# Performance work log

Measured on AMD Instinct MI355X. Metric: run time of the kernel, lower is better.

## Reference

```python
import jax, jax.numpy as jnp
import numpy as np

N, K, D = 262144, 1024, 64

def setup_inputs() -> dict:
    key = jax.random.key(0)
    kx, kc = jax.random.split(key)
    x = jax.random.normal(kx, (N, D), dtype=jnp.float32)
    centers = jax.random.normal(kc, (K, D), dtype=jnp.float32)
    return {"x": x, "centers": centers}

def reference(x, centers):
    # centers_norm is precomputed as a buffer in the torch module: (centers**2).sum(-1)
    centers_norm = jnp.sum(centers * centers, axis=-1)           # [K]
    x_norm = jnp.sum(x * x, axis=-1)                             # [N]
    dist = x_norm[..., None] - 2.0 * (x @ centers.T) + centers_norm  # [N,K]
    return jnp.argmin(jnp.abs(dist), axis=-1)                    # [N] int ids
```

## Files before the change

kernel.cpp:

```cpp
#include <hip/hip_runtime.h>
#include <float.h>


#define N_PTS 262144
#define K_CTR 1024
#define DIM   64
#define CTILE 128
#define OFFC  32.0f
#define TAU_DIST 0.05f

#define WS_CN    0
#define WS_CI    4096
#define WS_HI    8192
#define WS_LO    139264
#define WS_CTR   270336
#define WS_LIST  270592
#define WS_MIN   (270592 + 4 * 65536)

typedef __attribute__((ext_vector_type(8))) short  short8;
typedef __attribute__((ext_vector_type(8))) __bf16 bf16x8;
typedef __attribute__((ext_vector_type(4))) float  f32x4;

union FragU { short8 s; bf16x8 b; unsigned short u[8]; };

static __device__ __forceinline__ unsigned short bfbits(__bf16 h) {
    return __builtin_bit_cast(unsigned short, h);
}

#if defined(__has_builtin)
#if __has_builtin(__builtin_amdgcn_global_load_lds)
#define HAVE_GLD 1
#endif
#endif

#ifdef HAVE_GLD
#define GLD16(gsrc, ldst)                                                      \
    __builtin_amdgcn_global_load_lds(                                          \
        (const __attribute__((address_space(1))) void*)(gsrc),                 \
        (__attribute__((address_space(3))) void*)(ldst), 16, 0, 0)
#endif

__global__ void prep_kernel(const float* __restrict__ centers,
                            float* __restrict__ cn, float* __restrict__ ci,
                            int* __restrict__ counter) {
    int k = blockIdx.x * 256 + threadIdx.x;
    if (k == 0) *counter = 0;
    if (k < K_CTR) {
        const float4* c = reinterpret_cast<const float4*>(centers + (size_t)k * DIM);
        float s0 = 0.f, s1 = 0.f, s2 = 0.f, s3 = 0.f;
#pragma unroll
        for (int j = 0; j < 16; ++j) {
            float4 v = c[j];
            s0 = fmaf(v.x, v.x, s0); s1 = fmaf(v.y, v.y, s1);
            s2 = fmaf(v.z, v.z, s2); s3 = fmaf(v.w, v.w, s3);
        }
        float n = (s0 + s1) + (s2 + s3);
        cn[k] = n;
        ci[k] = fmaf(-0.5f, n, -OFFC);
    }
}

__global__ void split_kernel(const float* __restrict__ centers,
                             unsigned short* __restrict__ hiG,
                             unsigned short* __restrict__ loG) {
    int si = blockIdx.x * 256 + threadIdx.x;
    int rlow = si & 15, gg = (si >> 4) & 3, s = (si >> 6) & 1;
    int rowblk = (si >> 7) & 7, ct = si >> 10;
    int row = ct * CTILE + rowblk * 16 + rlow;
    const float* g = centers + (size_t)row * DIM + s * 32 + gg * 8;
    float4 v0 = *reinterpret_cast<const float4*>(g);
    float4 v1 = *reinterpret_cast<const float4*>(g + 4);
    float vv[8] = {v0.x, v0.y, v0.z, v0.w, v1.x, v1.y, v1.z, v1.w};
    FragU hi, lo;
#pragma unroll
    for (int j = 0; j < 8; ++j) {
        __bf16 h = (__bf16)vv[j];
        hi.u[j] = bfbits(h);
        lo.u[j] = bfbits((__bf16)(vv[j] - (float)h));
    }
    *reinterpret_cast<short8*>(hiG + (size_t)si * 8) = hi.s;
    *reinterpret_cast<short8*>(loG + (size_t)si * 8) = lo.s;
}

__launch_bounds__(256, 4)
__global__ void assign_mfma(const float* __restrict__ x,
                            const unsigned short* __restrict__ hiG,
                            const unsigned short* __restrict__ loG,
                            const float* __restrict__ ci,
                            int* __restrict__ out,
                            int* __restrict__ counter,
                            int* __restrict__ list, int cap) {
    __shared__ __align__(16) unsigned short lh[1024 * 8];
    __shared__ __align__(16) unsigned short ll[1024 * 8];
    __shared__ __align__(16) float ciL[K_CTR];

    const int tid  = threadIdx.x;
    const int wv   = tid >> 6;
    const int lane = tid & 63;
    const int g    = lane >> 4;
    const int lr   = lane & 15;
    const int pbase = blockIdx.x * 256 + wv * 64;

#pragma unroll
    for (int j = 0; j < 4; ++j) ciL[j * 256 + tid] = ci[j * 256 + tid];

    bf16x8 bh[4][2], bl[4][2];
#pragma unroll
    for (int cb = 0; cb < 4; ++cb) {
        const int p = pbase + cb * 16 + lr;
        const float* xr = x + (size_t)p * DIM + g * 8;
        float4 v0 = *reinterpret_cast<const float4*>(xr);
        float4 v1 = *reinterpret_cast<const float4*>(xr + 4);
        float4 v2 = *reinterpret_cast<const float4*>(xr + 32);
        float4 v3 = *reinterpret_cast<const float4*>(xr + 36);
        float vv[16] = {v0.x, v0.y, v0.z, v0.w, v1.x, v1.y, v1.z, v1.w,
                        v2.x, v2.y, v2.z, v2.w, v3.x, v3.y, v3.z, v3.w};
#pragma unroll
        for (int j = 0; j < 16; ++j) {
            __bf16 hb = (__bf16)vv[j];
            bh[cb][j >> 3][j & 7] = hb;
            bl[cb][j >> 3][j & 7] = (__bf16)(vv[j] - (float)hb);
        }
    }

    unsigned int best[4], sec[4];
#pragma unroll
    for (int cb = 0; cb < 4; ++cb) { best[cb] = 0xFFFFFFFFu; sec[cb] = 0xFFFFFFFFu; }

    const char* lhb = (const char*)lh + lane * 16;
    const char* llb = (const char*)ll + lane * 16;

#pragma unroll 1
    for (int ct = 0; ct < K_CTR / CTILE; ++ct) {
        __syncthreads();
        {
            const size_t sbase = (size_t)(ct * 1024 + wv * 64 + lane) * 8;
#ifdef HAVE_GLD
#pragma unroll
            for (int j = 0; j < 4; ++j) {
                GLD16(hiG + sbase + j * 256 * 8, lh + (j * 256 + wv * 64) * 8);
                GLD16(loG + sbase + j * 256 * 8, ll + (j * 256 + wv * 64) * 8);
            }
#else
            const short8* hs = reinterpret_cast<const short8*>(hiG + (size_t)ct * 1024 * 8);
            const short8* ls = reinterpret_cast<const short8*>(loG + (size_t)ct * 1024 * 8);
            short8* hd = reinterpret_cast<short8*>(lh);
            short8* ld = reinterpret_cast<short8*>(ll);
#pragma unroll
            for (int j = 0; j < 4; ++j) hd[j * 256 + tid] = hs[j * 256 + tid];
#pragma unroll
            for (int j = 0; j < 4; ++j) ld[j * 256 + tid] = ls[j * 256 + tid];
#endif
        }
        __syncthreads();

        const unsigned int ibct = ct * CTILE + g * 4;
        const float* cibase = ciL + ct * CTILE + g * 4;

#pragma unroll
        for (int st = 0; st < CTILE / 16; ++st) {
            FragU ah0, ah1, al0, al1;
            ah0.s = *reinterpret_cast<const short8*>(lhb + (st * 2 + 0) * 1024);
            ah1.s = *reinterpret_cast<const short8*>(lhb + (st * 2 + 1) * 1024);
            al0.s = *reinterpret_cast<const short8*>(llb + (st * 2 + 0) * 1024);
            al1.s = *reinterpret_cast<const short8*>(llb + (st * 2 + 1) * 1024);
            const f32x4 init4 = *reinterpret_cast<const f32x4*>(cibase + st * 16);

            f32x4 acc[4];
#pragma unroll
            for (int cb = 0; cb < 4; ++cb)
                acc[cb] = __builtin_amdgcn_mfma_f32_16x16x32_bf16(ah0.b, bh[cb][0], init4, 0, 0, 0);
#pragma unroll
            for (int cb = 0; cb < 4; ++cb)
                acc[cb] = __builtin_amdgcn_mfma_f32_16x16x32_bf16(ah0.b, bl[cb][0], acc[cb], 0, 0, 0);
#pragma unroll
            for (int cb = 0; cb < 4; ++cb)
                acc[cb] = __builtin_amdgcn_mfma_f32_16x16x32_bf16(al0.b, bh[cb][0], acc[cb], 0, 0, 0);
#pragma unroll
            for (int cb = 0; cb < 4; ++cb)
                acc[cb] = __builtin_amdgcn_mfma_f32_16x16x32_bf16(ah1.b, bh[cb][1], acc[cb], 0, 0, 0);
#pragma unroll
            for (int cb = 0; cb < 4; ++cb)
                acc[cb] = __builtin_amdgcn_mfma_f32_16x16x32_bf16(ah1.b, bl[cb][1], acc[cb], 0, 0, 0);
#pragma unroll
            for (int cb = 0; cb < 4; ++cb)
                acc[cb] = __builtin_amdgcn_mfma_f32_16x16x32_bf16(al1.b, bh[cb][1], acc[cb], 0, 0, 0);

            unsigned int vidx[4];
            vidx[0] = ibct + st * 16;
            vidx[1] = vidx[0] + 1; vidx[2] = vidx[0] + 2; vidx[3] = vidx[0] + 3;

#pragma unroll
            for (int cb = 0; cb < 4; ++cb) {
#pragma unroll
                for (int pr = 0; pr < 2; ++pr) {
                    unsigned int ka = (__float_as_uint(acc[cb][pr * 2 + 0]) & 0xFFFFFC00u) | vidx[pr * 2 + 0];
                    unsigned int kb = (__float_as_uint(acc[cb][pr * 2 + 1]) & 0xFFFFFC00u) | vidx[pr * 2 + 1];
                    unsigned int bo = best[cb], med, bn;
                    asm("v_med3_u32 %0, %1, %2, %3" : "=v"(med) : "v"(ka), "v"(kb), "v"(bo));
                    asm("v_min3_u32 %0, %1, %2, %3" : "=v"(bn)  : "v"(ka), "v"(kb), "v"(bo));
                    best[cb] = bn;
                    sec[cb]  = min(sec[cb], med);
                }
            }
        }
    }

#pragma unroll
    for (int cb = 0; cb < 4; ++cb) {
        unsigned int b = best[cb], s = sec[cb];
#pragma unroll
        for (int off = 16; off <= 32; off <<= 1) {
            unsigned int ob = __shfl_xor(b, off);
            unsigned int os = __shfl_xor(s, off);
            s = min(min(s, os), max(b, ob));
            b = min(b, ob);
        }
        if (g == 0) {
            const int p = pbase + cb * 16 + lr;
            out[p] = (int)(b & 1023u);
            float bf = __uint_as_float(b & 0xFFFFFC00u);
            float sf = __uint_as_float(s & 0xFFFFFC00u);
            if ((b < 0x80000000u) || (2.f * (bf - sf) < TAU_DIST)) {
                int sl = atomicAdd(counter, 1);
                if (sl < cap) list[sl] = p;
            }
        }
    }
}

__launch_bounds__(256, 2)
__global__ void refine2_kernel(const float* __restrict__ x,
                               const float* __restrict__ centers,
                               const float* __restrict__ cn,
                               const int* __restrict__ list,
                               const int* __restrict__ counter,
                               int* __restrict__ out, int cap) {
    __shared__ float ldsC[64 * 65];
    int cnt = *counter; if (cnt > cap) cnt = cap;
    const int tid  = threadIdx.x;
    const int wv   = tid >> 6;
    const int lane = tid & 63;

#pragma unroll 1
    for (int base = blockIdx.x * 4; base < cnt; base += gridDim.x * 4) {
        const int i = base + wv;
        const bool valid = (i < cnt);
        const int p = valid ? list[i] : 0;

        const float4* xr = reinterpret_cast<const float4*>(x + (size_t)p * DIM);
        float4 xv[16];
        float xn0 = 0.f, xn1 = 0.f, xn2 = 0.f, xn3 = 0.f;
#pragma unroll
        for (int j = 0; j < 16; ++j) {
            float4 v = xr[j]; xv[j] = v;
            xn0 = fmaf(v.x, v.x, xn0); xn1 = fmaf(v.y, v.y, xn1);
            xn2 = fmaf(v.z, v.z, xn2); xn3 = fmaf(v.w, v.w, xn3);
        }
        const float xnv = (xn0 + xn1) + (xn2 + xn3);

        float bestv = 3.4e38f; int bi = 0;
#pragma unroll 1
        for (int t = 0; t < 16; ++t) {
            __syncthreads();
#pragma unroll
            for (int j = 0; j < 16; ++j) {
                int idx = j * 256 + tid;
                int row = idx >> 6, col = idx & 63;
                ldsC[row * 65 + col] = centers[((size_t)t * 64 + row) * DIM + col];
            }
            __syncthreads();
            if (valid) {
                const int k = t * 64 + lane;
                const float* cr = ldsC + lane * 65;
                float a0 = 0.f, a1 = 0.f, a2 = 0.f, a3 = 0.f;
#pragma unroll
                for (int jj = 0; jj < 16; ++jj) {
                    a0 = fmaf(xv[jj].x, cr[jj * 4 + 0], a0);
                    a1 = fmaf(xv[jj].y, cr[jj * 4 + 1], a1);
                    a2 = fmaf(xv[jj].z, cr[jj * 4 + 2], a2);
                    a3 = fmaf(xv[jj].w, cr[jj * 4 + 3], a3);
                }
                float dot  = (a0 + a1) + (a2 + a3);
                float dist = fabsf(fmaf(-2.f, dot, xnv + cn[k]));
                if (dist < bestv) { bestv = dist; bi = k; }
            }
        }
#pragma unroll
        for (int off = 1; off < 64; off <<= 1) {
            float ob = __shfl_xor(bestv, off);
            int   oi = __shfl_xor(bi, off);
            bool take = (ob < bestv) || (ob == bestv && oi < bi);
            bestv = take ? ob : bestv;
            bi    = take ? oi : bi;
        }
        if (valid && lane == 0) out[p] = bi;
    }
}

#define TK 128
__launch_bounds__(256, 4)
__global__ void assign_fp32(const float* __restrict__ x,
                            const float* __restrict__ centers,
                            const float* __restrict__ cn,
                            int* __restrict__ out) {
    __shared__ float ldsC[TK * DIM];
    __shared__ float ldsN[TK];
    const int tid = threadIdx.x;
    const int p = blockIdx.x * 256 + tid;
    const float4* xr = reinterpret_cast<const float4*>(x + (size_t)p * DIM);
    float4 xv[16];
    float xn0 = 0.f, xn1 = 0.f, xn2 = 0.f, xn3 = 0.f;
#pragma unroll
    for (int j = 0; j < 16; ++j) {
        float4 v = xr[j]; xv[j] = v;
        xn0 = fmaf(v.x, v.x, xn0); xn1 = fmaf(v.y, v.y, xn1);
        xn2 = fmaf(v.z, v.z, xn2); xn3 = fmaf(v.w, v.w, xn3);
    }
    const float xn = (xn0 + xn1) + (xn2 + xn3);
    float bestv = 3.4e38f; int best = 0;
#pragma unroll 1
    for (int t = 0; t < K_CTR / TK; ++t) {
        __syncthreads();
        const float4* cg = reinterpret_cast<const float4*>(centers + (size_t)t * TK * DIM);
        float4* cl = reinterpret_cast<float4*>(ldsC);
#pragma unroll
        for (int j = 0; j < (TK * DIM / 4) / 256; ++j)
            cl[j * 256 + tid] = cg[j * 256 + tid];
        if (tid < TK) ldsN[tid] = cn[t * TK + tid];
        __syncthreads();
        for (int k = 0; k < TK; ++k) {
            const float4* cv = reinterpret_cast<const float4*>(ldsC + k * DIM);
            float a0 = 0.f, a1 = 0.f, a2 = 0.f, a3 = 0.f;
#pragma unroll
            for (int j = 0; j < 16; ++j) {
                float4 c4 = cv[j];
                a0 = fmaf(xv[j].x, c4.x, a0); a1 = fmaf(xv[j].y, c4.y, a1);
                a2 = fmaf(xv[j].z, c4.z, a2); a3 = fmaf(xv[j].w, c4.w, a3);
            }
            float dot = (a0 + a1) + (a2 + a3);
            float dist = fabsf(fmaf(-2.f, dot, xn + ldsN[k]));
            if (dist < bestv) { bestv = dist; best = t * TK + k; }
        }
    }
    out[p] = best;
}

extern "C" void kernel_launch(void* const* d_in, const int* in_sizes, int n_in,
                              void* d_out, int out_size, void* d_ws, size_t ws_size,
                              hipStream_t stream) {
    const float* x = (const float*)d_in[0];
    const float* centers = (const float*)d_in[1];
    int* out = (int*)d_out;
    char* ws = (char*)d_ws;
    float* cn = (float*)(ws + WS_CN);
    float* ci = (float*)(ws + WS_CI);
    unsigned short* hiG = (unsigned short*)(ws + WS_HI);
    unsigned short* loG = (unsigned short*)(ws + WS_LO);
    int* counter = (int*)(ws + WS_CTR);
    int* list = (int*)(ws + WS_LIST);

    if (ws_size >= WS_MIN) {
        size_t avail = (ws_size - WS_LIST) / sizeof(int);
        int cap = (int)(avail < (size_t)N_PTS ? avail : (size_t)N_PTS);
        prep_kernel<<<4, 256, 0, stream>>>(centers, cn, ci, counter);
        split_kernel<<<32, 256, 0, stream>>>(centers, hiG, loG);
        assign_mfma<<<N_PTS / 256, 256, 0, stream>>>(x, hiG, loG, ci, out, counter, list, cap);
        refine2_kernel<<<1024, 256, 0, stream>>>(x, centers, cn, list, counter, out, cap);
    } else {
        prep_kernel<<<4, 256, 0, stream>>>(centers, cn, ci, counter);
        assign_fp32<<<N_PTS / 256, 256, 0, stream>>>(x, centers, cn, out);
    }
}
```

Before: 120.1 us.

## Double-buffer center tiles in LDS and raise MFMA wave priority

Halves the center tile to 64 rows and double-buffers the hi/lo bf16 fragments in shared memory, so the next tile is fetched while the current one feeds the MFMAs. This drops one barrier per iteration and overlaps global-to-LDS loads with compute. It also wraps the MFMA block in s_setprio to favour waves issuing matrix ops. The split kernel's layout changes to match the new tile size. Twice as many loop iterations add per-tile overhead, while total LDS use stays about the same.

```diff
diff --git a/kernel.cpp b/kernel.cpp
--- a/kernel.cpp
+++ b/kernel.cpp
@@ -5,7 +5,8 @@
 #define N_PTS 262144
 #define K_CTR 1024
 #define DIM   64
-#define CTILE 128
+#define CTILE 64
+#define NTILE (K_CTR / CTILE)
 #define OFFC  32.0f
 #define TAU_DIST 0.05f
 
@@ -64,10 +65,10 @@
                              unsigned short* __restrict__ hiG,
                              unsigned short* __restrict__ loG) {
     int si = blockIdx.x * 256 + threadIdx.x;
-    int rlow = si & 15, gg = (si >> 4) & 3, s = (si >> 6) & 1;
-    int rowblk = (si >> 7) & 7, ct = si >> 10;
-    int row = ct * CTILE + rowblk * 16 + rlow;
-    const float* g = centers + (size_t)row * DIM + s * 32 + gg * 8;
+    int lane = si & 63, ks = (si >> 6) & 1, st = (si >> 7) & 3, tile = si >> 9;
+    int row = tile * CTILE + st * 16 + (lane & 15);
+    int dimb = ks * 32 + ((lane >> 4) & 3) * 8;
+    const float* g = centers + (size_t)row * DIM + dimb;
     float4 v0 = *reinterpret_cast<const float4*>(g);
     float4 v1 = *reinterpret_cast<const float4*>(g + 4);
     float vv[8] = {v0.x, v0.y, v0.z, v0.w, v1.x, v1.y, v1.z, v1.w};
@@ -90,8 +91,8 @@
                             int* __restrict__ out,
                             int* __restrict__ counter,
                             int* __restrict__ list, int cap) {
-    __shared__ __align__(16) unsigned short lh[1024 * 8];
-    __shared__ __align__(16) unsigned short ll[1024 * 8];
+    __shared__ __align__(16) unsigned short lh[2 * 512 * 8];
+    __shared__ __align__(16) unsigned short ll[2 * 512 * 8];
     __shared__ __align__(16) float ciL[K_CTR];
 
     const int tid  = threadIdx.x;
@@ -127,46 +128,54 @@
 #pragma unroll
     for (int cb = 0; cb < 4; ++cb) { best[cb] = 0xFFFFFFFFu; sec[cb] = 0xFFFFFFFFu; }
 
-    const char* lhb = (const char*)lh + lane * 16;
-    const char* llb = (const char*)ll + lane * 16;
-
+#define STAGE(buf, tile)                                                       \
+    do {                                                                       \
+        const size_t sb = (size_t)((tile) * 512 + wv * 64 + lane) * 8;         \
+        unsigned short* dh = lh + ((buf) * 512 + wv * 64) * 8;                 \
+        unsigned short* dl = ll + ((buf) * 512 + wv * 64) * 8;                 \
+        GLD16(hiG + sb, dh);                                                   \
+        GLD16(hiG + sb + 256 * 8, dh + 256 * 8);                               \
+        GLD16(loG + sb, dl);                                                   \
+        GLD16(loG + sb + 256 * 8, dl + 256 * 8);                               \
+    } while (0)
+
+#ifndef HAVE_GLD
+#undef STAGE
+#define STAGE(buf, tile)                                                       \
+    do {                                                                       \
+        const short8* hs = reinterpret_cast<const short8*>(hiG) + (tile) * 512; \
+        const short8* ls = reinterpret_cast<const short8*>(loG) + (tile) * 512; \
+        short8* hd = reinterpret_cast<short8*>(lh) + (buf) * 512;              \
+        short8* ld = reinterpret_cast<short8*>(ll) + (buf) * 512;              \
+        hd[tid] = hs[tid]; hd[256 + tid] = hs[256 + tid];                      \
+        ld[tid] = ls[tid]; ld[256 + tid] = ls[256 + tid];                      \
+    } while (0)
+#endif
+
+    STAGE(0, 0);
+    __syncthreads();
+
+    int cur = 0;
 #pragma unroll 1
-    for (int ct = 0; ct < K_CTR / CTILE; ++ct) {
-        __syncthreads();
-        {
-            const size_t sbase = (size_t)(ct * 1024 + wv * 64 + lane) * 8;
-#ifdef HAVE_GLD
-#pragma unroll
-            for (int j = 0; j < 4; ++j) {
-                GLD16(hiG + sbase + j * 256 * 8, lh + (j * 256 + wv * 64) * 8);
-                GLD16(loG + sbase + j * 256 * 8, ll + (j * 256 + wv * 64) * 8);
-            }
-#else
-            const short8* hs = reinterpret_cast<const short8*>(hiG + (size_t)ct * 1024 * 8);
-            const short8* ls = reinterpret_cast<const short8*>(loG + (size_t)ct * 1024 * 8);
-            short8* hd = reinterpret_cast<short8*>(lh);
-            short8* ld = reinterpret_cast<short8*>(ll);
-#pragma unroll
-            for (int j = 0; j < 4; ++j) hd[j * 256 + tid] = hs[j * 256 + tid];
-#pragma unroll
-            for (int j = 0; j < 4; ++j) ld[j * 256 + tid] = ls[j * 256 + tid];
-#endif
-        }
-        __syncthreads();
-
-        const unsigned int ibct = ct * CTILE + g * 4;
-        const float* cibase = ciL + ct * CTILE + g * 4;
+    for (int tile = 0; tile < NTILE; ++tile) {
+        if (tile < NTILE - 1) STAGE(cur ^ 1, tile + 1);
+
+        const char* lhc = (const char*)lh + cur * 512 * 16 + lane * 16;
+        const char* llc = (const char*)ll + cur * 512 * 16 + lane * 16;
+        const unsigned int ibt = tile * CTILE + g * 4;
+        const float* cib = ciL + tile * CTILE + g * 4;
 
 #pragma unroll
         for (int st = 0; st < CTILE / 16; ++st) {
             FragU ah0, ah1, al0, al1;
-            ah0.s = *reinterpret_cast<const short8*>(lhb + (st * 2 + 0) * 1024);
-            ah1.s = *reinterpret_cast<const short8*>(lhb + (st * 2 + 1) * 1024);
-            al0.s = *reinterpret_cast<const short8*>(llb + (st * 2 + 0) * 1024);
-            al1.s = *reinterpret_cast<const short8*>(llb + (st * 2 + 1) * 1024);
-            const f32x4 init4 = *reinterpret_cast<const f32x4*>(cibase + st * 16);
+            ah0.s = *reinterpret_cast<const short8*>(lhc + st * 2048);
+            ah1.s = *reinterpret_cast<const short8*>(lhc + st * 2048 + 1024);
+            al0.s = *reinterpret_cast<const short8*>(llc + st * 2048);
+            al1.s = *reinterpret_cast<const short8*>(llc + st * 2048 + 1024);
+            const f32x4 init4 = *reinterpret_cast<const f32x4*>(cib + st * 16);
 
             f32x4 acc[4];
+            __builtin_amdgcn_s_setprio(1);
 #pragma unroll
             for (int cb = 0; cb < 4; ++cb)
                 acc[cb] = __builtin_amdgcn_mfma_f32_16x16x32_bf16(ah0.b, bh[cb][0], init4, 0, 0, 0);
@@ -185,9 +194,10 @@
 #pragma unroll
             for (int cb = 0; cb < 4; ++cb)
                 acc[cb] = __builtin_amdgcn_mfma_f32_16x16x32_bf16(al1.b, bh[cb][1], acc[cb], 0, 0, 0);
+            __builtin_amdgcn_s_setprio(0);
 
             unsigned int vidx[4];
-            vidx[0] = ibct + st * 16;
+            vidx[0] = ibt + st * 16;
             vidx[1] = vidx[0] + 1; vidx[2] = vidx[0] + 2; vidx[3] = vidx[0] + 3;
 
 #pragma unroll
@@ -204,6 +214,9 @@
                 }
             }
         }
+
+        __syncthreads();
+        cur ^= 1;
     }
 
 #pragma unroll
```

Result: no change. 119.0 us (-0.9%).
